# Optimization experiments

Hardware: AMD Instinct MI355X
Metric: run time of the kernel (lower is better)

Reference implementation:

```python
import jax, jax.numpy as jnp
import numpy as np
from jax.ops import segment_sum

N_NODES = 50000
N_EDGES = 800000
D = 128
N_LAYERS = 3
N_GRAPHS = 256


def setup_inputs() -> dict:
    key = jax.random.key(0)
    k1, k2, k3, k4, k5, k6 = jax.random.split(key, 6)
    feats = jax.random.normal(k1, (N_NODES, D), dtype=jnp.float32)
    src = jax.random.randint(k2, (N_EDGES,), 0, N_NODES)
    dst = jax.random.randint(k3, (N_EDGES,), 0, N_NODES)
    graph_ids = jnp.sort(jax.random.randint(k4, (N_NODES,), 0, N_GRAPHS))
    W = jax.random.normal(k5, (N_LAYERS, D, D), dtype=jnp.float32) / np.float32(np.sqrt(D))
    b = jax.random.normal(k6, (N_LAYERS, D), dtype=jnp.float32) * 0.01
    return {"feats": feats, "W": W, "b": b, "src": src, "dst": dst, "graph_ids": graph_ids}


def reference(feats, W, b, src, dst, graph_ids):
    # DGL GraphConv with norm='both': h' = act(D_in^{-1/2} A D_out^{-1/2} h W + b)
    ones_e = jnp.ones((src.shape[0],), dtype=feats.dtype)
    deg_out = jnp.clip(segment_sum(ones_e, src, num_segments=N_NODES), 1.0)  # [N]
    deg_in = jnp.clip(segment_sum(ones_e, dst, num_segments=N_NODES), 1.0)   # [N]
    norm_out = jax.lax.rsqrt(deg_out)[:, None]  # [N,1]
    norm_in = jax.lax.rsqrt(deg_in)[:, None]    # [N,1]

    h = feats
    for l in range(N_LAYERS):
        hn = h * norm_out                                  # source-side norm
        agg = segment_sum(hn[src], dst, num_segments=N_NODES)  # SpMM gather/scatter
        agg = agg * norm_in                                # dest-side norm
        h = jax.nn.relu(agg @ W[l] + b[l])                 # [N,D]

    # AvgPooling readout: per-graph mean over nodes
    ones_n = jnp.ones((N_NODES,), dtype=h.dtype)
    counts = jnp.clip(segment_sum(ones_n, graph_ids, num_segments=N_GRAPHS), 1.0)
    pooled = segment_sum(h, graph_ids, num_segments=N_GRAPHS) / counts[:, None]
    return pooled  # [N_GRAPHS, D]
```

## Files before the change

kernel.cpp:

```cpp
#include <hip/hip_runtime.h>
#include <hip/hip_fp16.h>

#define DD 128
#define GG 256
#define RANGES 8
#define RSMAX 6400
#define NCHUNK 32

typedef _Float16 half8 __attribute__((ext_vector_type(8)));
typedef float floatx4 __attribute__((ext_vector_type(4)));

__device__ inline uint2 pack_half4(float4 v) {
    __half2 a = __floats2half2_rn(v.x, v.y);
    __half2 b = __floats2half2_rn(v.z, v.w);
    uint2 u;
    u.x = *reinterpret_cast<unsigned int*>(&a);
    u.y = *reinterpret_cast<unsigned int*>(&b);
    return u;
}

__global__ __launch_bounds__(256) void k_hist2(const int* __restrict__ src, const int* __restrict__ dst,
                                               int* __restrict__ pout, int* __restrict__ pin,
                                               int E, int N, int C, int RS, int L) {
    __shared__ int ho[RSMAX];
    __shared__ int hi[RSMAX];
    int r = blockIdx.x / C;
    int c = blockIdx.x % C;
    int r0 = r * RS;
    int r1 = min(r0 + RS, N);
    int nb = r1 - r0;
    for (int i = threadIdx.x; i < nb; i += 256) { ho[i] = 0; hi[i] = 0; }
    __syncthreads();
    int e0 = c * L, e1 = min(e0 + L, E);
    for (int e = e0 + threadIdx.x * 4; e < e1; e += 1024) {
        if (e + 3 < e1) {
            int4 s4 = *(const int4*)&src[e];
            int4 d4 = *(const int4*)&dst[e];
            if (s4.x >= r0 && s4.x < r1) atomicAdd(&ho[s4.x - r0], 1);
            if (s4.y >= r0 && s4.y < r1) atomicAdd(&ho[s4.y - r0], 1);
            if (s4.z >= r0 && s4.z < r1) atomicAdd(&ho[s4.z - r0], 1);
            if (s4.w >= r0 && s4.w < r1) atomicAdd(&ho[s4.w - r0], 1);
            if (d4.x >= r0 && d4.x < r1) atomicAdd(&hi[d4.x - r0], 1);
            if (d4.y >= r0 && d4.y < r1) atomicAdd(&hi[d4.y - r0], 1);
            if (d4.z >= r0 && d4.z < r1) atomicAdd(&hi[d4.z - r0], 1);
            if (d4.w >= r0 && d4.w < r1) atomicAdd(&hi[d4.w - r0], 1);
        } else {
            for (int j = 0; j < 4 && e + j < e1; ++j) {
                int s = src[e + j], d = dst[e + j];
                if (s >= r0 && s < r1) atomicAdd(&ho[s - r0], 1);
                if (d >= r0 && d < r1) atomicAdd(&hi[d - r0], 1);
            }
        }
    }
    __syncthreads();
    for (int i = threadIdx.x; i < nb; i += 256) {
        pout[(size_t)c * N + r0 + i] = ho[i];
        pin[(size_t)c * N + r0 + i] = hi[i];
    }
}

__global__ void k_reduce(const int* __restrict__ pout, const int* __restrict__ pin,
                         float* __restrict__ norm_out, float* __restrict__ norm_in,
                         int* __restrict__ deg_in, int N, int C) {
    int n = blockIdx.x * blockDim.x + threadIdx.x;
    if (n >= N) return;
    int so = 0, si = 0;
    for (int c = 0; c < C; ++c) {
        so += pout[(size_t)c * N + n];
        si += pin[(size_t)c * N + n];
    }
    norm_out[n] = rsqrtf(fmaxf((float)so, 1.0f));
    norm_in[n] = rsqrtf(fmaxf((float)si, 1.0f));
    deg_in[n] = si;
}

__global__ void k_base(const int* __restrict__ pin, const int* __restrict__ row_ptr,
                       int* __restrict__ base, int N, int C) {
    int n = blockIdx.x * blockDim.x + threadIdx.x;
    if (n >= N) return;
    int run = row_ptr[n];
    for (int c = 0; c < C; ++c) {
        int h = pin[(size_t)c * N + n];
        base[(size_t)c * N + n] = run;
        run += h;
    }
}

__global__ void k_gstart(const int* __restrict__ gid, int* g_start, int N, int G) {
    int g = blockIdx.x * blockDim.x + threadIdx.x;
    if (g > G) return;
    int lo = 0, hi = N;
    while (lo < hi) {
        int mid = (lo + hi) >> 1;
        if (gid[mid] < g) lo = mid + 1; else hi = mid;
    }
    g_start[g] = lo;
}

__global__ __launch_bounds__(256) void k_scan_a(const int* __restrict__ deg, int* bsum, int n) {
    __shared__ int wsum[4];
    int base = blockIdx.x * 1024 + threadIdx.x * 4;
    int s = 0;
    #pragma unroll
    for (int j = 0; j < 4; ++j) s += (base + j < n) ? deg[base + j] : 0;
    #pragma unroll
    for (int off = 32; off; off >>= 1) s += __shfl_xor(s, off);
    int lane = threadIdx.x & 63, w = threadIdx.x >> 6;
    if (lane == 0) wsum[w] = s;
    __syncthreads();
    if (threadIdx.x == 0) bsum[blockIdx.x] = wsum[0] + wsum[1] + wsum[2] + wsum[3];
}

__global__ void k_scan_b(int* bsum, int nblk, int* row_ptr, int n) {
    int lane = threadIdx.x;
    int carry = 0;
    for (int base = 0; base < nblk; base += 64) {
        int i = base + lane;
        int v = (i < nblk) ? bsum[i] : 0;
        int s = v;
        #pragma unroll
        for (int off = 1; off < 64; off <<= 1) {
            int u = __shfl_up(s, off);
            if (lane >= off) s += u;
        }
        if (i < nblk) bsum[i] = carry + s - v;
        carry += __shfl(s, 63);
    }
    if (lane == 0) row_ptr[n] = carry;
}

__global__ __launch_bounds__(256) void k_scan_c(const int* __restrict__ deg, const int* __restrict__ bsum,
                                                int* row_ptr, int n) {
    __shared__ int wsum[4];
    int t = threadIdx.x;
    int base = blockIdx.x * 1024 + t * 4;
    int v[4];
    #pragma unroll
    for (int j = 0; j < 4; ++j) v[j] = (base + j < n) ? deg[base + j] : 0;
    int ts = v[0] + v[1] + v[2] + v[3];
    int lane = t & 63, w = t >> 6;
    int incl = ts;
    #pragma unroll
    for (int off = 1; off < 64; off <<= 1) {
        int u = __shfl_up(incl, off);
        if (lane >= off) incl += u;
    }
    if (lane == 63) wsum[w] = incl;
    __syncthreads();
    int woff = 0;
    for (int j = 0; j < w; ++j) woff += wsum[j];
    int run = bsum[blockIdx.x] + woff + incl - ts;
    #pragma unroll
    for (int j = 0; j < 4; ++j) {
        if (base + j < n) row_ptr[base + j] = run;
        run += v[j];
    }
}

__global__ __launch_bounds__(256) void k_fill2(const int* __restrict__ src, const int* __restrict__ dst,
                                               const int* __restrict__ base, int* __restrict__ col_src,
                                               int E, int N, int C, int RS, int L) {
    __shared__ int cnt[RSMAX];
    int r = blockIdx.x / C;
    int c = blockIdx.x % C;
    int r0 = r * RS;
    int r1 = min(r0 + RS, N);
    int nb = r1 - r0;
    const int* bc = base + (size_t)c * N;
    for (int i = threadIdx.x; i < nb; i += 256) cnt[i] = bc[r0 + i];
    __syncthreads();
    int e0 = c * L, e1 = min(e0 + L, E);
    for (int e = e0 + threadIdx.x * 4; e < e1; e += 1024) {
        if (e + 3 < e1) {
            int4 s4 = *(const int4*)&src[e];
            int4 d4 = *(const int4*)&dst[e];
            if (d4.x >= r0 && d4.x < r1) { int o = atomicAdd(&cnt[d4.x - r0], 1); col_src[o] = s4.x; }
            if (d4.y >= r0 && d4.y < r1) { int o = atomicAdd(&cnt[d4.y - r0], 1); col_src[o] = s4.y; }
            if (d4.z >= r0 && d4.z < r1) { int o = atomicAdd(&cnt[d4.z - r0], 1); col_src[o] = s4.z; }
            if (d4.w >= r0 && d4.w < r1) { int o = atomicAdd(&cnt[d4.w - r0], 1); col_src[o] = s4.w; }
        } else {
            for (int j = 0; j < 4 && e + j < e1; ++j) {
                int s = src[e + j], d = dst[e + j];
                if (d >= r0 && d < r1) { int o = atomicAdd(&cnt[d - r0], 1); col_src[o] = s; }
            }
        }
    }
}

__global__ void k_wconv(const float* __restrict__ W, __half* __restrict__ Wt) {
    int i = blockIdx.x * blockDim.x + threadIdx.x;
    if (i >= 3 * 16384) return;
    int l = i >> 14;
    int rem = i & 16383;
    int n = rem >> 7;
    int k = rem & 127;
    Wt[(size_t)l * 16384 + n * 128 + k] = __float2half(W[(size_t)l * 16384 + k * 128 + n]);
}

__global__ void k_scale(const float* __restrict__ h, const float* __restrict__ norm_out,
                        uint2* __restrict__ Xh, int N) {
    int i = blockIdx.x * blockDim.x + threadIdx.x;
    if (i < N * 32) {
        int n = i >> 5;
        float4 v = ((const float4*)h)[i];
        float s = norm_out[n];
        v.x *= s; v.y *= s; v.z *= s; v.w *= s;
        Xh[i] = pack_half4(v);
    }
}

__device__ inline void acc_row(float* acc, uint4 u) {
    const __half2* h = (const __half2*)&u;
    #pragma unroll
    for (int i = 0; i < 4; ++i) {
        float2 f = __half22float2(h[i]);
        acc[2 * i] += f.x;
        acc[2 * i + 1] += f.y;
    }
}

__global__ __launch_bounds__(256, 8) void k_agg(const uint4* __restrict__ Xin, const float* __restrict__ norm_in,
                                                const int* __restrict__ row_ptr, const int* __restrict__ col_src,
                                                uint4* __restrict__ Yh, int N) {
    int t = threadIdx.x;
    int l16 = t & 15;
    int n = blockIdx.x * 16 + (t >> 4);
    if (n >= N) return;
    int beg = row_ptr[n], end = row_ptr[n + 1];
    float acc[8] = {};
    int k = beg;
    for (; k + 3 < end; k += 4) {
        int4 s = *(const int4*)&col_src[k];
        uint4 u0 = Xin[(size_t)s.x * 16 + l16];
        uint4 u1 = Xin[(size_t)s.y * 16 + l16];
        uint4 u2 = Xin[(size_t)s.z * 16 + l16];
        uint4 u3 = Xin[(size_t)s.w * 16 + l16];
        acc_row(acc, u0);
        acc_row(acc, u1);
        acc_row(acc, u2);
        acc_row(acc, u3);
    }
    for (; k < end; ++k) {
        uint4 u = Xin[(size_t)col_src[k] * 16 + l16];
        acc_row(acc, u);
    }
    float ni = norm_in[n];
    #pragma unroll
    for (int i = 0; i < 8; ++i) acc[i] *= ni;
    __half2 hp[4];
    #pragma unroll
    for (int i = 0; i < 4; ++i) hp[i] = __floats2half2_rn(acc[2 * i], acc[2 * i + 1]);
    Yh[(size_t)n * 16 + l16] = *(uint4*)hp;
}

__global__ __launch_bounds__(256) void k_mm_mfma(const __half* __restrict__ Yh, const __half* __restrict__ Wt,
                                                 const float* __restrict__ bl, const float* __restrict__ scale,
                                                 float* __restrict__ outf, __half* __restrict__ outh, int N) {
    __shared__ _Float16 Ah[64 * 136];
    __shared__ _Float16 Bt[128 * 136];
    int tid = threadIdx.x;
    int n0 = blockIdx.x * 64;

    for (int q = tid; q < 1024; q += 256) {
        int r = q >> 4, c = q & 15;
        int node = n0 + r;
        float4 v = make_float4(0.f, 0.f, 0.f, 0.f);
        if (node < N) v = *(const float4*)&Yh[(size_t)node * 128 + c * 8];
        *(float4*)&Ah[r * 136 + c * 8] = v;
    }
    for (int q = tid; q < 2048; q += 256) {
        int r = q >> 4, c = q & 15;
        *(float4*)&Bt[r * 136 + c * 8] = *(const float4*)&Wt[(size_t)r * 128 + c * 8];
    }
    __syncthreads();

    int wave = tid >> 6;
    int lane = tid & 63;
    int quad = lane >> 4;
    int mrow = lane & 15;
    int m0 = wave * 16;

    half8 af[4];
    #pragma unroll
    for (int kc = 0; kc < 4; ++kc)
        af[kc] = *(const half8*)&Ah[(m0 + mrow) * 136 + kc * 32 + quad * 8];

    floatx4 acc[8];
    #pragma unroll
    for (int ct = 0; ct < 8; ++ct) acc[ct] = (floatx4){0.f, 0.f, 0.f, 0.f};

    #pragma unroll
    for (int ct = 0; ct < 8; ++ct) {
        #pragma unroll
        for (int kc = 0; kc < 4; ++kc) {
            half8 bf = *(const half8*)&Bt[(ct * 16 + mrow) * 136 + kc * 32 + quad * 8];
            acc[ct] = __builtin_amdgcn_mfma_f32_16x16x32_f16(af[kc], bf, acc[ct], 0, 0, 0);
        }
    }

    float sc[4];
    #pragma unroll
    for (int r = 0; r < 4; ++r) {
        int node = n0 + m0 + quad * 4 + r;
        sc[r] = (scale && node < N) ? scale[node] : 1.0f;
    }
    #pragma unroll
    for (int ct = 0; ct < 8; ++ct) {
        int col = ct * 16 + mrow;
        float bias = bl[col];
        #pragma unroll
        for (int r = 0; r < 4; ++r) {
            int node = n0 + m0 + quad * 4 + r;
            if (node < N) {
                float val = fmaxf(acc[ct][r] + bias, 0.f);
                if (outh) outh[(size_t)node * 128 + col] = __float2half(val * sc[r]);
                else outf[(size_t)node * 128 + col] = val;
            }
        }
    }
}

__global__ __launch_bounds__(128) void k_pool(const float* __restrict__ h, const int* __restrict__ g_start,
                                              float* __restrict__ out) {
    int g = blockIdx.x;
    int t = threadIdx.x;
    int beg = g_start[g], end = g_start[g + 1];
    float acc = 0.0f;
    int n = beg;
    for (; n + 3 < end; n += 4) {
        float a0 = h[(size_t)n * DD + t];
        float a1 = h[(size_t)(n + 1) * DD + t];
        float a2 = h[(size_t)(n + 2) * DD + t];
        float a3 = h[(size_t)(n + 3) * DD + t];
        acc += a0 + a1 + a2 + a3;
    }
    for (; n < end; ++n) acc += h[(size_t)n * DD + t];
    float cnt = (float)(end - beg);
    out[(size_t)g * DD + t] = acc / fmaxf(cnt, 1.0f);
}

extern "C" void kernel_launch(void* const* d_in, const int* in_sizes, int n_in,
                              void* d_out, int out_size, void* d_ws, size_t ws_size,
                              hipStream_t stream) {
    const float* feats = (const float*)d_in[0];
    const float* W = (const float*)d_in[1];
    const float* b = (const float*)d_in[2];
    const int* src = (const int*)d_in[3];
    const int* dst = (const int*)d_in[4];
    const int* gid = (const int*)d_in[5];
    float* out = (float*)d_out;
    const int N = in_sizes[0] / DD;
    const int E = in_sizes[3];

    const int C = NCHUNK;
    const int RS = (N + RANGES - 1) / RANGES;
    const int L = (((E + C - 1) / C) + 3) & ~3;

    char* ws = (char*)d_ws;
    size_t off = 0;
    auto take = [&](size_t bytes) {
        char* p = ws + off;
        off = (off + bytes + 255) & ~(size_t)255;
        return p;
    };
    float* norm_out = (float*)take((size_t)N * 4);
    float* norm_in  = (float*)take((size_t)N * 4);
    int*   deg_in   = (int*)take((size_t)N * 4);
    int*   row_ptr  = (int*)take((size_t)(N + 1) * 4);
    int*   col_src  = (int*)take((size_t)E * 4);
    int*   g_start  = (int*)take((size_t)(GG + 1) * 4);
    int*   bsum     = (int*)take((size_t)1024 * 4);
    __half* Wth     = (__half*)take((size_t)3 * 16384 * 2);
    uint4* Xh       = (uint4*)take((size_t)N * DD * 2);
    uint4* Yh       = (uint4*)take((size_t)N * DD * 2);
    size_t part_bytes = 3 * ((size_t)C * N * 4 + 256);
    size_t f_bytes = (size_t)N * DD * 4;
    char* uni = take(part_bytes > f_bytes ? part_bytes : f_bytes);
    int* pout  = (int*)uni;
    int* pin   = (int*)(uni + (((size_t)C * N * 4 + 255) & ~(size_t)255));
    int* fbase = (int*)(uni + 2 * (((size_t)C * N * 4 + 255) & ~(size_t)255));
    float* F   = (float*)uni;

    const int nblk = (N + 1023) / 1024;

    k_hist2<<<RANGES * C, 256, 0, stream>>>(src, dst, pout, pin, E, N, C, RS, L);
    k_reduce<<<(N + 255) / 256, 256, 0, stream>>>(pout, pin, norm_out, norm_in, deg_in, N, C);
    k_gstart<<<1, 512, 0, stream>>>(gid, g_start, N, GG);
    k_wconv<<<(3 * 16384 + 255) / 256, 256, 0, stream>>>(W, Wth);
    k_scan_a<<<nblk, 256, 0, stream>>>(deg_in, bsum, N);
    k_scan_b<<<1, 64, 0, stream>>>(bsum, nblk, row_ptr, N);
    k_scan_c<<<nblk, 256, 0, stream>>>(deg_in, bsum, row_ptr, N);
    k_base<<<(N + 255) / 256, 256, 0, stream>>>(pin, row_ptr, fbase, N, C);
    k_fill2<<<RANGES * C, 256, 0, stream>>>(src, dst, fbase, col_src, E, N, C, RS, L);

    k_scale<<<(N * 32 + 255) / 256, 256, 0, stream>>>(feats, norm_out, (uint2*)Xh, N);

    const int agrid = (N + 15) / 16;
    const int mgrid = (N + 63) / 64;
    for (int l = 0; l < 3; ++l) {
        k_agg<<<agrid, 256, 0, stream>>>(Xh, norm_in, row_ptr, col_src, Yh, N);
        const __half* Wtl = Wth + (size_t)l * 16384;
        const float* bl = b + (size_t)l * DD;
        if (l < 2)
            k_mm_mfma<<<mgrid, 256, 0, stream>>>((const __half*)Yh, Wtl, bl, norm_out,
                                                 nullptr, (__half*)Xh, N);
        else
            k_mm_mfma<<<mgrid, 256, 0, stream>>>((const __half*)Yh, Wtl, bl, nullptr,
                                                 F, nullptr, N);
    }
    k_pool<<<GG, 128, 0, stream>>>(F, g_start, out);
}
```

Baseline: 320.1 us.

## Pack degree histograms into 16-bit pairs, prefetch agg indices, store final layer in fp16

```diff
diff --git a/kernel.cpp b/kernel.cpp
--- a/kernel.cpp
+++ b/kernel.cpp
@@ -20,7 +20,7 @@
 }
 
 __global__ __launch_bounds__(256) void k_hist2(const int* __restrict__ src, const int* __restrict__ dst,
-                                               int* __restrict__ pout, int* __restrict__ pin,
+                                               unsigned int* __restrict__ pk,
                                                int E, int N, int C, int RS, int L) {
     __shared__ int ho[RSMAX];
     __shared__ int hi[RSMAX];
@@ -53,34 +53,33 @@
         }
     }
     __syncthreads();
-    for (int i = threadIdx.x; i < nb; i += 256) {
-        pout[(size_t)c * N + r0 + i] = ho[i];
-        pin[(size_t)c * N + r0 + i] = hi[i];
-    }
-}
-
-__global__ void k_reduce(const int* __restrict__ pout, const int* __restrict__ pin,
+    for (int i = threadIdx.x; i < nb; i += 256)
+        pk[(size_t)c * N + r0 + i] = (unsigned int)ho[i] | ((unsigned int)hi[i] << 16);
+}
+
+__global__ void k_reduce(const unsigned int* __restrict__ pk,
                          float* __restrict__ norm_out, float* __restrict__ norm_in,
                          int* __restrict__ deg_in, int N, int C) {
     int n = blockIdx.x * blockDim.x + threadIdx.x;
     if (n >= N) return;
     int so = 0, si = 0;
     for (int c = 0; c < C; ++c) {
-        so += pout[(size_t)c * N + n];
-        si += pin[(size_t)c * N + n];
+        unsigned int v = pk[(size_t)c * N + n];
+        so += (int)(v & 0xFFFFu);
+        si += (int)(v >> 16);
     }
     norm_out[n] = rsqrtf(fmaxf((float)so, 1.0f));
     norm_in[n] = rsqrtf(fmaxf((float)si, 1.0f));
     deg_in[n] = si;
 }
 
-__global__ void k_base(const int* __restrict__ pin, const int* __restrict__ row_ptr,
+__global__ void k_base(const unsigned int* __restrict__ pk, const int* __restrict__ row_ptr,
                        int* __restrict__ base, int N, int C) {
     int n = blockIdx.x * blockDim.x + threadIdx.x;
     if (n >= N) return;
     int run = row_ptr[n];
     for (int c = 0; c < C; ++c) {
-        int h = pin[(size_t)c * N + n];
+        int h = (int)(pk[(size_t)c * N + n] >> 16);
         base[(size_t)c * N + n] = run;
         run += h;
     }
@@ -229,8 +228,14 @@
     int beg = row_ptr[n], end = row_ptr[n + 1];
     float acc[8] = {};
     int k = beg;
-    for (; k + 3 < end; k += 4) {
-        int4 s = *(const int4*)&col_src[k];
+    bool have = (k + 3 < end);
+    int4 s;
+    if (have) s = *(const int4*)&col_src[k];
+    while (have) {
+        int kn = k + 4;
+        bool haven = (kn + 3 < end);
+        int4 sn = s;
+        if (haven) sn = *(const int4*)&col_src[kn];
         uint4 u0 = Xin[(size_t)s.x * 16 + l16];
         uint4 u1 = Xin[(size_t)s.y * 16 + l16];
         uint4 u2 = Xin[(size_t)s.z * 16 + l16];
@@ -239,6 +244,7 @@
         acc_row(acc, u1);
         acc_row(acc, u2);
         acc_row(acc, u3);
+        s = sn; k = kn; have = haven;
     }
     for (; k < end; ++k) {
         uint4 u = Xin[(size_t)col_src[k] * 16 + l16];
@@ -320,23 +326,30 @@
     }
 }
 
-__global__ __launch_bounds__(128) void k_pool(const float* __restrict__ h, const int* __restrict__ g_start,
+__global__ __launch_bounds__(256) void k_pool(const __half2* __restrict__ Fh, const int* __restrict__ g_start,
                                               float* __restrict__ out) {
+    __shared__ float2 red[4][64];
     int g = blockIdx.x;
     int t = threadIdx.x;
+    int cp = t & 63;
+    int nl = t >> 6;
     int beg = g_start[g], end = g_start[g + 1];
-    float acc = 0.0f;
-    int n = beg;
-    for (; n + 3 < end; n += 4) {
-        float a0 = h[(size_t)n * DD + t];
-        float a1 = h[(size_t)(n + 1) * DD + t];
-        float a2 = h[(size_t)(n + 2) * DD + t];
-        float a3 = h[(size_t)(n + 3) * DD + t];
-        acc += a0 + a1 + a2 + a3;
-    }
-    for (; n < end; ++n) acc += h[(size_t)n * DD + t];
-    float cnt = (float)(end - beg);
-    out[(size_t)g * DD + t] = acc / fmaxf(cnt, 1.0f);
+    float2 acc = make_float2(0.f, 0.f);
+    for (int n = beg + nl; n < end; n += 4) {
+        float2 f = __half22float2(Fh[(size_t)n * 64 + cp]);
+        acc.x += f.x;
+        acc.y += f.y;
+    }
+    red[nl][cp] = acc;
+    __syncthreads();
+    if (nl == 0) {
+        float2 a0 = red[0][cp], a1 = red[1][cp], a2 = red[2][cp], a3 = red[3][cp];
+        float cnt = fmaxf((float)(end - beg), 1.0f);
+        float2 o;
+        o.x = (a0.x + a1.x + a2.x + a3.x) / cnt;
+        o.y = (a0.y + a1.y + a2.y + a3.y) / cnt;
+        *(float2*)&out[(size_t)g * DD + cp * 2] = o;
+    }
 }
 
 extern "C" void kernel_launch(void* const* d_in, const int* in_sizes, int n_in,
@@ -373,24 +386,24 @@
     __half* Wth     = (__half*)take((size_t)3 * 16384 * 2);
     uint4* Xh       = (uint4*)take((size_t)N * DD * 2);
     uint4* Yh       = (uint4*)take((size_t)N * DD * 2);
-    size_t part_bytes = 3 * ((size_t)C * N * 4 + 256);
-    size_t f_bytes = (size_t)N * DD * 4;
-    char* uni = take(part_bytes > f_bytes ? part_bytes : f_bytes);
-    int* pout  = (int*)uni;
-    int* pin   = (int*)(uni + (((size_t)C * N * 4 + 255) & ~(size_t)255));
-    int* fbase = (int*)(uni + 2 * (((size_t)C * N * 4 + 255) & ~(size_t)255));
-    float* F   = (float*)uni;
+    size_t chunk_arr = ((size_t)C * N * 4 + 255) & ~(size_t)255;
+    size_t uni_bytes = 2 * chunk_arr;
+    size_t fh_bytes = (size_t)N * DD * 2;
+    char* uni = take(uni_bytes > fh_bytes ? uni_bytes : fh_bytes);
+    unsigned int* pk = (unsigned int*)uni;
+    int* fbase = (int*)(uni + chunk_arr);
+    __half* Fh = (__half*)uni;
 
     const int nblk = (N + 1023) / 1024;
 
-    k_hist2<<<RANGES * C, 256, 0, stream>>>(src, dst, pout, pin, E, N, C, RS, L);
-    k_reduce<<<(N + 255) / 256, 256, 0, stream>>>(pout, pin, norm_out, norm_in, deg_in, N, C);
+    k_hist2<<<RANGES * C, 256, 0, stream>>>(src, dst, pk, E, N, C, RS, L);
+    k_reduce<<<(N + 255) / 256, 256, 0, stream>>>(pk, norm_out, norm_in, deg_in, N, C);
     k_gstart<<<1, 512, 0, stream>>>(gid, g_start, N, GG);
     k_wconv<<<(3 * 16384 + 255) / 256, 256, 0, stream>>>(W, Wth);
     k_scan_a<<<nblk, 256, 0, stream>>>(deg_in, bsum, N);
     k_scan_b<<<1, 64, 0, stream>>>(bsum, nblk, row_ptr, N);
     k_scan_c<<<nblk, 256, 0, stream>>>(deg_in, bsum, row_ptr, N);
-    k_base<<<(N + 255) / 256, 256, 0, stream>>>(pin, row_ptr, fbase, N, C);
+    k_base<<<(N + 255) / 256, 256, 0, stream>>>(pk, row_ptr, fbase, N, C);
     k_fill2<<<RANGES * C, 256, 0, stream>>>(src, dst, fbase, col_src, E, N, C, RS, L);
 
     k_scale<<<(N * 32 + 255) / 256, 256, 0, stream>>>(feats, norm_out, (uint2*)Xh, N);
@@ -406,7 +419,7 @@
                                                  nullptr, (__half*)Xh, N);
         else
             k_mm_mfma<<<mgrid, 256, 0, stream>>>((const __half*)Yh, Wtl, bl, nullptr,
-                                                 F, nullptr, N);
-    }
-    k_pool<<<GG, 128, 0, stream>>>(F, g_start, out);
-}
+                                                 nullptr, Fh, N);
+    }
+    k_pool<<<GG, 256, 0, stream>>>((const __half2*)Fh, g_start, out);
+}
```

Result: faster. 313.5 us (-2.1%).
